# Optimization experiments

Hardware: AMD Instinct MI355X
Metric: run time of the kernel (lower is better)

The kernel has to match this reference:

```python
import jax, jax.numpy as jnp
import numpy as np
from jax import lax

IMG = 224.0
IOU_THRESH = 0.5

def box_cxcywh_to_xyxy(b):
    cx, cy, w, h = b[..., 0], b[..., 1], b[..., 2], b[..., 3]
    return jnp.stack([cx - 0.5 * w, cy - 0.5 * h, cx + 0.5 * w, cy + 0.5 * h], axis=-1)

def box_iou(a, b):
    area_a = (a[:, 2] - a[:, 0]) * (a[:, 3] - a[:, 1])
    area_b = (b[:, 2] - b[:, 0]) * (b[:, 3] - b[:, 1])
    lt = jnp.maximum(a[:, None, :2], b[None, :, :2])
    rb = jnp.minimum(a[:, None, 2:], b[None, :, 2:])
    wh = jnp.clip(rb - lt, 0.0)
    inter = wh[..., 0] * wh[..., 1]
    return inter / (area_a[:, None] + area_b[None, :] - inter)

def gumbel_softmax(key, logits, axis, tau=1.0):
    # straight-through hard gumbel-softmax (matches torch hard=True)
    g = jax.random.gumbel(key, logits.shape, logits.dtype)
    y = jax.nn.softmax((logits + g) / tau, axis=axis)
    y_hard = jax.nn.one_hot(jnp.argmax(y, axis=axis), y.shape[axis], axis=axis, dtype=y.dtype)
    return y + lax.stop_gradient(y_hard - y)

def nms_indices(boxes, scores, thresh):
    # iterative greedy NMS, returns kept indices in descending-score order (as torchvision)
    n = boxes.shape[0]
    order = jnp.argsort(-scores)
    b = boxes[order]
    areas = (b[:, 2] - b[:, 0]) * (b[:, 3] - b[:, 1])
    pos = jnp.arange(n)
    def body(i, suppressed):
        bi = b[i]
        lt = jnp.maximum(bi[:2], b[:, :2])
        rb = jnp.minimum(bi[2:], b[:, 2:])
        wh = jnp.clip(rb - lt, 0.0)
        inter = wh[:, 0] * wh[:, 1]
        iou = inter / (areas[i] + areas - inter)
        sup = (iou > thresh) & (pos > i) & jnp.logical_not(suppressed[i])
        return suppressed | sup
    suppressed = lax.fori_loop(0, n, body, jnp.zeros((n,), bool))
    keep = np.asarray(jnp.logical_not(suppressed))
    return jnp.asarray(np.asarray(order)[keep])

def _keys():
    return jax.random.split(jax.random.key(42), 3)

def _boxes_and_scores(classencodings, pred_logits, pred_boxes, tgt_ids, batch_idx, tgt_bbox, k0):
    C = classencodings.shape[0]
    B, Q, D = pred_logits.shape
    similarity = jnp.einsum('bqd,cd->bqc', pred_logits, classencodings)
    out_scores = jnp.max(similarity, axis=-1)
    clt = gumbel_softmax(k0, similarity, axis=-1)                      # [B,Q,C] hard
    offx = jnp.arange(C, dtype=pred_logits.dtype) * IMG
    offy = jnp.arange(B, dtype=pred_logits.dtype) * IMG
    ox = jnp.sum(clt * offx, axis=-1)                                  # [B,Q]
    oy = jnp.broadcast_to(offy[:, None], (B, Q))
    out_off = jnp.tile(jnp.stack([ox, oy], axis=-1), (1, 1, 2))        # [B,Q,4]
    out_bbox = (box_cxcywh_to_xyxy(pred_boxes) + out_off).reshape(-1, 4)
    f = pred_logits.dtype
    gt_off = jnp.tile(jnp.stack([IMG * tgt_ids.astype(f), IMG * batch_idx.astype(f)], axis=-1), (1, 2))
    tb = box_cxcywh_to_xyxy(tgt_bbox) + gt_off                         # [N,4]
    return similarity, out_scores.reshape(-1), out_bbox, tb

def ce_diag(logits):
    # CrossEntropyLoss(mean) with targets arange(n)
    return -jnp.mean(jnp.diagonal(jax.nn.log_softmax(logits, axis=1)))

def _forward(classencodings, pred_logits, pred_boxes, pred_masks, tgt_masks, tgt_embs, tgt_bbox, tgt_ids, batch_idx, nms_idx):
    k0, k1, k2 = _keys()
    B, Q, D = pred_logits.shape
    N = tgt_embs.shape[0]
    W, H = tgt_masks.shape[-2:]
    similarity, out_scores, out_bbox, tb = _boxes_and_scores(classencodings, pred_logits, pred_boxes, tgt_ids, batch_idx, tgt_bbox, k0)
    kept = out_bbox[nms_idx]                                           # [K,4]
    K = kept.shape[0]
    iou = box_iou(kept, tb)
    iou = jnp.where(jnp.isnan(iou), 0.0, iou)
    gt_log = jax.nn.softmax(iou, axis=1)
    gt_one_hot = gumbel_softmax(k1, gt_log, axis=1)                    # [K,N]
    gt_sel = gt_one_hot.T @ kept                                       # [N,4]
    gt_ious = jnp.diagonal(box_iou(gt_sel, tb))
    out_embs = gt_one_hot.T @ pred_logits.reshape(-1, D)[nms_idx]      # [N,D]
    class_loss = ce_diag(tgt_embs @ out_embs.T) + ce_diag(out_embs @ tgt_embs.T)
    scores = jnp.einsum('bqd,nd->bqn', pred_logits, tgt_embs).reshape(B * Q, N)
    ind = gumbel_softmax(k2, scores, axis=0).T                         # [N,B*Q]
    om = (ind @ pred_masks.reshape(B * Q, -1)).reshape(N, W, H)
    overall_mask_loss = jnp.mean((om - tgt_masks) ** 2)
    ocm = jnp.einsum('qwh,bcq->bcwh', om, similarity) / om.shape[1]    # [B,Q,W,H] (N==C==Q)
    ocm = jax.nn.softmax(ocm, axis=1)
    batch_lookup = jax.nn.one_hot(batch_idx, B, dtype=pred_logits.dtype).T  # [B,N]
    gt_sim = tgt_embs @ classencodings.T                               # [N,C]
    tsim = batch_lookup[:, :, None] * gt_sim[None, :, :]               # [B,N,C]
    gt_cm = jnp.einsum('bnc,nwh->bcwh', tsim, tgt_masks)               # [B,C,W,H]
    inp = ocm.reshape(B, -1)
    tgt = gt_cm.reshape(B, -1)
    dice = jnp.mean(jnp.sum(inp * tgt) / (jnp.sum(inp, -1) + jnp.sum(tgt, -1) + 1e-6))
    l1 = jnp.abs(gt_sel - tb).sum()
    return jnp.stack([class_loss, dice, overall_mask_loss / K, (1.0 - gt_ious).sum() / K, l1 / K])

def setup_inputs():
    key = jax.random.key(0)
    ks = jax.random.split(key, 10)
    B, Q, C, N, D, W, H = 8, 300, 300, 300, 256, 96, 96
    return {
        'classencodings': jax.random.normal(ks[0], (C, D), jnp.float32),
        'pred_logits': jax.random.normal(ks[1], (B, Q, D), jnp.float32),
        'pred_boxes': jax.random.uniform(ks[2], (B, Q, 4), jnp.float32),
        'pred_masks': jax.random.normal(ks[3], (B * Q, W, H), jnp.float32),
        'tgt_masks': jax.random.uniform(ks[4], (N, W, H), jnp.float32),
        'tgt_embs': jax.random.normal(ks[5], (N, D), jnp.float32),
        'tgt_bbox': jax.random.uniform(ks[6], (N, 4), jnp.float32),
        'im_masks': jnp.ones((B, 224, 224), jnp.float32),
        'tgt_ids': jax.random.randint(ks[7], (N,), 0, C, jnp.int32),
        'batch_idx': jnp.sort(jax.random.randint(ks[8], (N,), 0, B, jnp.int32)),
    }

def reference(classencodings, pred_logits, pred_boxes, pred_masks, tgt_masks, tgt_embs, tgt_bbox, im_masks, tgt_ids, batch_idx):
    k0, _, _ = _keys()
    _, scores, out_bbox, _ = _boxes_and_scores(classencodings, pred_logits, pred_boxes, tgt_ids, batch_idx, tgt_bbox, k0)
    nms_idx = nms_indices(out_bbox, scores, IOU_THRESH)
    return _forward(classencodings, pred_logits, pred_boxes, pred_masks, tgt_masks, tgt_embs, tgt_bbox, tgt_ids, batch_idx, nms_idx)
```

## Files before the change

### kernel.cpp

```cpp
#include <hip/hip_runtime.h>
#include <stdint.h>

#define DEVFN __device__ __forceinline__

typedef unsigned short u16;
typedef short bf16x8 __attribute__((ext_vector_type(8)));
typedef float f32x4 __attribute__((ext_vector_type(4)));

constexpr int BB = 8, QQ = 300, CC = 300, NN = 300, DD = 256;
constexpr int WHX = 9216, BQ = 2400, SIMW = 600;
constexpr int QP = 320;
constexpr int CP = 304;
constexpr int KP = 96;
constexpr int NP = 416;
constexpr int CELLCAP = 300;

constexpr size_t F_SIMS   = 0;
constexpr size_t F_GTSIM  = F_SIMS   + (size_t)BQ*SIMW;
constexpr size_t F_MM     = F_GTSIM  + (size_t)NN*CC;
constexpr size_t F_SCORE  = F_MM     + (size_t)NN*NN;
constexpr size_t F_BBOX   = F_SCORE  + BQ;
constexpr size_t F_TB     = F_BBOX   + (size_t)BQ*4;
constexpr size_t F_SB     = F_TB     + (size_t)NN*4;
constexpr size_t F_SAREA  = F_SB     + (size_t)BQ*4;
constexpr size_t F_KB     = F_SAREA  + BQ;
constexpr size_t F_ROWSUM = F_KB     + (size_t)BQ*4;
constexpr size_t F_OE     = F_ROWSUM + NN;
constexpr size_t F_GSEL   = F_OE     + (size_t)NN*DD;
constexpr size_t F_MSUM   = F_GSEL   + (size_t)NN*4;
constexpr size_t F_STGT   = F_MSUM   + NN;
constexpr size_t F_SC     = F_STGT   + 8;
constexpr size_t F_CNT    = F_SC     + 16;
constexpr size_t F_ACCEND = F_CNT    + BQ;
constexpr size_t F_ORDER  = F_ACCEND;
constexpr size_t F_NMSIDX = F_ORDER  + BQ;
constexpr size_t F_SEL2   = F_NMSIDX + BQ;
constexpr size_t F_BSTART = F_SEL2   + NN;
constexpr size_t F_KINT   = F_BSTART + 16;
constexpr size_t F_CLS    = F_KINT   + 4;
constexpr size_t F_KEEPF  = F_CLS    + BQ;
constexpr size_t F_LIST   = F_KEEPF  + BQ;
constexpr size_t F_SIMTB  = ((F_LIST + (size_t)BQ*CELLCAP + 7) & ~(size_t)7);
constexpr size_t F_OMT    = F_SIMTB + (size_t)BB*CP*QP/2;
constexpr size_t F_TMT    = F_OMT   + (size_t)WHX*QP/2;
constexpr size_t F_GTP    = F_TMT   + (size_t)WHX*NP/2;
constexpr size_t F_TOTAL  = F_GTP   + (size_t)BB*CP*KP/2;

DEVFN uint32_t rotl32(uint32_t v, int r){ return (v << r) | (v >> (32 - r)); }

DEVFN void tf2x32(uint32_t k0, uint32_t k1, uint32_t x0, uint32_t x1,
                  uint32_t& o0, uint32_t& o1){
  uint32_t ks2 = k0 ^ k1 ^ 0x1BD11BDAu;
  x0 += k0; x1 += k1;
#define TFR(r) x0 += x1; x1 = rotl32(x1, r); x1 ^= x0;
  TFR(13) TFR(15) TFR(26) TFR(6)   x0 += k1;  x1 += ks2 + 1u;
  TFR(17) TFR(29) TFR(16) TFR(24)  x0 += ks2; x1 += k0  + 2u;
  TFR(13) TFR(15) TFR(26) TFR(6)   x0 += k0;  x1 += k1  + 3u;
  TFR(17) TFR(29) TFR(16) TFR(24)  x0 += k1;  x1 += ks2 + 4u;
  TFR(13) TFR(15) TFR(26) TFR(6)   x0 += ks2; x1 += k0  + 5u;
#undef TFR
  o0 = x0; o1 = x1;
}

DEVFN void subkey(int i, uint32_t& k0, uint32_t& k1){
  tf2x32(0u, 42u, 0u, (uint32_t)i, k0, k1);
}

DEVFN float gumbel32(uint32_t k0, uint32_t k1, uint32_t idx){
  uint32_t h, l; tf2x32(k0, k1, 0u, idx, h, l);
  uint32_t bits = h ^ l;
  float f = __uint_as_float((bits >> 9) | 0x3F800000u) - 1.0f;
  const float tiny = 1.17549435e-38f;
  float u = fmaxf(tiny, f + tiny);
  return -logf(-logf(u));
}

DEVFN float iou_xyxy(float ax1,float ay1,float ax2,float ay2,
                     float bx1,float by1,float bx2,float by2){
  float aa = (ax2-ax1)*(ay2-ay1);
  float ab = (bx2-bx1)*(by2-by1);
  float lx = fmaxf(ax1,bx1), ly = fmaxf(ay1,by1);
  float rx = fminf(ax2,bx2), ry = fminf(ay2,by2);
  float iw = fmaxf(rx-lx,0.f), ih = fmaxf(ry-ly,0.f);
  float in_ = iw*ih;
  return in_/(aa+ab-in_);
}

DEVFN u16 f2bf(float x){
  uint32_t u = __float_as_uint(x);
  uint32_t r = u + 0x7FFFu + ((u >> 16) & 1u);
  return (u16)(r >> 16);
}

DEVFN void gload_lds16(const u16* g, u16* l){
  __builtin_amdgcn_global_load_lds(
      (const __attribute__((address_space(1))) unsigned int*)g,
      (__attribute__((address_space(3))) unsigned int*)l,
      16, 0, 0);
}

__global__ __launch_bounds__(256) void k_gemm_t(
    const float* __restrict__ pl, const float* __restrict__ ce,
    const float* __restrict__ te, float* __restrict__ sims,
    float* __restrict__ gtsim){
  __shared__ float As[16][64];
  __shared__ float Bs[16][64];
  const int row0 = blockIdx.x * 64, col0 = blockIdx.y * 64;
  const int tid = threadIdx.x;
  const int lrow = tid >> 2, lk0 = (tid & 3) * 4;
  const int tr = tid >> 4, tc = tid & 15;

  float acc[4][4];
  #pragma unroll
  for (int i = 0; i < 4; i++)
    #pragma unroll
    for (int j = 0; j < 4; j++) acc[i][j] = 0.f;

  const float4 z4 = {0.f,0.f,0.f,0.f};
  const int grow = row0 + lrow;
  const int gcol = col0 + lrow;
  const float* arow = nullptr;
  if (grow < 2400) arow = pl + (size_t)grow * DD;
  else if (grow < 2700) arow = te + (size_t)(grow - 2400) * DD;
  const float* brow = nullptr;
  if (gcol < 300) brow = ce + (size_t)gcol * DD;
  else if (gcol < 600) brow = te + (size_t)(gcol - 300) * DD;

  float4 av = arow ? *(const float4*)(arow + lk0) : z4;
  float4 bv = brow ? *(const float4*)(brow + lk0) : z4;

  for (int step = 0; step < 16; step++){
    __syncthreads();
    #pragma unroll
    for (int j = 0; j < 4; j++){
      As[lk0 + j][lrow] = ((const float*)&av)[j];
      Bs[lk0 + j][lrow] = ((const float*)&bv)[j];
    }
    __syncthreads();
    if (step + 1 < 16){
      const int k0 = (step + 1) * 16;
      av = arow ? *(const float4*)(arow + k0 + lk0) : z4;
      bv = brow ? *(const float4*)(brow + k0 + lk0) : z4;
    }
    #pragma unroll
    for (int kk = 0; kk < 16; kk++){
      float4 a4 = *(const float4*)&As[kk][tr*4];
      float4 b4 = *(const float4*)&Bs[kk][tc*4];
      float a[4] = {a4.x,a4.y,a4.z,a4.w};
      float b[4] = {b4.x,b4.y,b4.z,b4.w};
      #pragma unroll
      for (int i = 0; i < 4; i++)
        #pragma unroll
        for (int j = 0; j < 4; j++)
          acc[i][j] = fmaf(a[i], b[j], acc[i][j]);
    }
  }

  #pragma unroll
  for (int i = 0; i < 4; i++){
    const int r = row0 + tr*4 + i;
    const int c0 = col0 + tc*4;
    if (r < 2400){
      if (c0 < 600){
        float4 o0 = {acc[i][0],acc[i][1],acc[i][2],acc[i][3]};
        *(float4*)(sims + (size_t)r*SIMW + c0) = o0;
      }
    } else if (r < 2700){
      const int n = r - 2400;
      #pragma unroll
      for (int j = 0; j < 4; j++){
        int c = c0 + j;
        if (c < 300) gtsim[(size_t)n*CC + c] = acc[i][j];
      }
    }
  }
}

__global__ __launch_bounds__(512) void k_post(
    const float* __restrict__ sims, const float* __restrict__ pb,
    const float* __restrict__ tbb, const int* __restrict__ tids,
    const int* __restrict__ bidx, const float* __restrict__ gtsim,
    float* __restrict__ score, float* __restrict__ bbox,
    float* __restrict__ tb, float* __restrict__ rowsum,
    int* __restrict__ clsout){
  int bq = blockIdx.x, tid = threadIdx.x;
  __shared__ float sv[512];
  __shared__ int   si[512];
  float v = (tid < CC) ? sims[(size_t)bq*SIMW + tid] : -INFINITY;
  sv[tid] = v; __syncthreads();
  for (int s = 256; s > 0; s >>= 1){ if (tid < s) sv[tid] = fmaxf(sv[tid], sv[tid+s]); __syncthreads(); }
  if (tid == 0) score[bq] = sv[0];
  __syncthreads();
  uint32_t gk0, gk1; subkey(0, gk0, gk1);
  float y = (tid < CC) ? v + gumbel32(gk0, gk1, (uint32_t)(bq*CC + tid)) : -INFINITY;
  sv[tid] = y; si[tid] = tid; __syncthreads();
  for (int s = 256; s > 0; s >>= 1){
    if (tid < s){
      float ov = sv[tid+s]; int oi = si[tid+s];
      if (ov > sv[tid] || (ov == sv[tid] && oi < si[tid])){ sv[tid] = ov; si[tid] = oi; }
    }
    __syncthreads();
  }
  if (tid == 0){
    int cls = si[0];
    clsout[bq] = cls;
    float ox = 224.0f * (float)cls;
    float oy = 224.0f * (float)(bq / QQ);
    float cx = pb[bq*4+0], cy = pb[bq*4+1], ww = pb[bq*4+2], hh = pb[bq*4+3];
    bbox[bq*4+0] = cx - 0.5f*ww + ox;
    bbox[bq*4+1] = cy - 0.5f*hh + oy;
    bbox[bq*4+2] = cx + 0.5f*ww + ox;
    bbox[bq*4+3] = cy + 0.5f*hh + oy;
  }
  if (bq < NN){
    __syncthreads();
    float rs = (tid < CC) ? gtsim[(size_t)bq*CC + tid] : 0.f;
    sv[tid] = rs; __syncthreads();
    for (int s = 256; s > 0; s >>= 1){ if (tid < s) sv[tid] += sv[tid+s]; __syncthreads(); }
    if (tid == 0) rowsum[bq] = sv[0];
    if (tid == 1){
      float gx = 224.0f * (float)tids[bq], gy = 224.0f * (float)bidx[bq];
      float cx = tbb[bq*4+0], cy = tbb[bq*4+1], ww = tbb[bq*4+2], hh = tbb[bq*4+3];
      tb[bq*4+0] = cx - 0.5f*ww + gx;
      tb[bq*4+1] = cy - 0.5f*hh + gy;
      tb[bq*4+2] = cx + 0.5f*ww + gx;
      tb[bq*4+3] = cy + 0.5f*hh + gy;
    }
  }
}

__global__ __launch_bounds__(256) void k_rankgather(
    const float* __restrict__ score, const float* __restrict__ bbox,
    const int* __restrict__ cls, const int* __restrict__ bidx,
    int* __restrict__ order, float* __restrict__ sb,
    int* __restrict__ bstart, int* __restrict__ cnt,
    int* __restrict__ list){
  const int t = blockIdx.x;
  const int tid = threadIdx.x;
  const float st = score[t];
  int c = 0;
  for (int j = tid; j < BQ; j += 256){
    float sj = score[j];
    c += (sj > st) || (sj == st && j < t);
  }
  __shared__ int red[256];
  red[tid] = c; __syncthreads();
  for (int s = 128; s > 0; s >>= 1){
    if (tid < s) red[tid] += red[tid+s];
    __syncthreads();
  }
  if (tid == 0){
    int r = red[0];
    order[r] = t;
    float x1 = bbox[t*4+0], y1 = bbox[t*4+1], x2 = bbox[t*4+2], y2 = bbox[t*4+3];
    sb[r*4+0] = x1; sb[r*4+1] = y1; sb[r*4+2] = x2; sb[r*4+3] = y2;
    int key = (t / QQ) * CC + cls[t];
    int slot = atomicAdd(&cnt[key], 1);
    list[(size_t)key*CELLCAP + slot] = r;
  }
  if (t == 0 && tid >= 32 && tid < 41){
    int b = tid - 32, cb = 0;
    for (int n = 0; n < NN; n++) cb += (bidx[n] < b);
    bstart[b] = cb;
  }
}

__global__ __launch_bounds__(256) void k_cellnms(
    const float* __restrict__ sb, const int* __restrict__ cnt,
    const int* __restrict__ list, int* __restrict__ keepf){
  int key = blockIdx.x*256 + threadIdx.x;
  if (key >= BB*CC) return;
  int m = cnt[key];
  if (m <= 0) return;
  const int* lst = list + (size_t)key*CELLCAP;
  unsigned long long keptmask = 0ull;
  int prevp = -1;
  for (int a = 0; a < m; a++){
    int pa = 0x7fffffff;
    for (int j = 0; j < m; j++){
      int pj = lst[j];
      if (pj > prevp && pj < pa) pa = pj;
    }
    prevp = pa;
    float4 A = ((const float4*)sb)[pa];
    float areaA = (A.z-A.x)*(A.w-A.y);
    bool kept = true;
    int pbprev = -1;
    for (int b2 = 0; b2 < a; b2++){
      int pb = 0x7fffffff;
      for (int j = 0; j < m; j++){
        int pj = lst[j];
        if (pj > pbprev && pj < pb) pb = pj;
      }
      pbprev = pb;
      bool keptb = (m <= 64) ? (((keptmask >> b2) & 1ull) != 0ull) : (keepf[pb] != 0);
      if (!keptb) continue;
      float4 B = ((const float4*)sb)[pb];
      float areaB = (B.z-B.x)*(B.w-B.y);
      float lx = fmaxf(A.x,B.x), ly = fmaxf(A.y,B.y);
      float rx = fminf(A.z,B.z), ry = fminf(A.w,B.w);
      float iw = fmaxf(rx-lx,0.f), ih = fmaxf(ry-ly,0.f);
      float inter = iw*ih;
      if (inter/(areaA + areaB - inter) > 0.5f){ kept = false; break; }
    }
    if (m <= 64 && kept) keptmask |= (1ull << a);
    keepf[pa] = kept ? 1 : 0;
  }
}

__global__ __launch_bounds__(256) void k_compact(
    const int* __restrict__ keepflag, const int* __restrict__ order,
    const float* __restrict__ sb, int* __restrict__ nmsidx,
    float* __restrict__ kb, int* __restrict__ kint){
  __shared__ int csum[256];
  int tid = threadIdx.x;
  int p0 = tid*10;
  int keepf[10];
  int cnt = 0;
  #pragma unroll
  for (int d = 0; d < 10; d++){
    int p = p0 + d;
    int k = 0;
    if (p < BQ) k = keepflag[p];
    keepf[d] = k; cnt += k;
  }
  csum[tid] = cnt; __syncthreads();
  for (int s = 1; s < 256; s <<= 1){
    int add = (tid >= s) ? csum[tid - s] : 0;
    __syncthreads();
    csum[tid] += add;
    __syncthreads();
  }
  int pos = csum[tid] - cnt;
  #pragma unroll
  for (int d = 0; d < 10; d++){
    if (keepf[d]){
      int p = p0 + d;
      nmsidx[pos] = order[p];
      ((float4*)kb)[pos] = ((const float4*)sb)[p];
      pos++;
    }
  }
  if (tid == 255) kint[0] = csum[255];
}

__global__ __launch_bounds__(512) void k_gtsel(
    const float* __restrict__ kb, const float* __restrict__ tb,
    const int* __restrict__ nmsidx, const float* __restrict__ pl,
    const int* __restrict__ kint, float* __restrict__ gsel,
    float* __restrict__ oe){
  int k = blockIdx.x;
  if (k >= kint[0]) return;
  int tid = threadIdx.x;
  __shared__ float sv[512];
  __shared__ int   si[512];
  float4 a = ((const float4*)kb)[k];
  float iou = -INFINITY;
  if (tid < NN){
    float4 t = ((const float4*)tb)[tid];
    iou = iou_xyxy(a.x,a.y,a.z,a.w, t.x,t.y,t.z,t.w);
    if (iou != iou) iou = 0.f;
  }
  sv[tid] = iou; __syncthreads();
  for (int s = 256; s > 0; s >>= 1){ if (tid < s) sv[tid] = fmaxf(sv[tid], sv[tid+s]); __syncthreads(); }
  float m = sv[0]; __syncthreads();
  float e = (tid < NN) ? expf(iou - m) : 0.f;
  sv[tid] = e; __syncthreads();
  for (int s = 256; s > 0; s >>= 1){ if (tid < s) sv[tid] += sv[tid+s]; __syncthreads(); }
  float S = sv[0]; __syncthreads();
  uint32_t gk0, gk1; subkey(1, gk0, gk1);
  float y = (tid < NN) ? (e / S + gumbel32(gk0, gk1, (uint32_t)(k*NN + tid))) : -INFINITY;
  sv[tid] = y; si[tid] = tid; __syncthreads();
  for (int s = 256; s > 0; s >>= 1){
    if (tid < s){
      float ov = sv[tid+s]; int oi = si[tid+s];
      if (ov > sv[tid] || (ov == sv[tid] && oi < si[tid])){ sv[tid] = ov; si[tid] = oi; }
    }
    __syncthreads();
  }
  int sel = si[0];
  if (tid < 4) atomicAdd(&gsel[sel*4 + tid], ((const float*)&a)[tid]);
  if (tid < DD) atomicAdd(&oe[(size_t)sel*DD + tid], pl[(size_t)nmsidx[k]*DD + tid]);
}

__global__ __launch_bounds__(256) void k_m(
    const float* __restrict__ te, const float* __restrict__ oe,
    float* __restrict__ M){
  int idx = blockIdx.x*256 + threadIdx.x;
  if (idx >= NN*NN) return;
  int i = idx / NN, j = idx % NN;
  const float4* a4 = (const float4*)(te + (size_t)i*DD);
  const float4* b4 = (const float4*)(oe + (size_t)j*DD);
  float s = 0.f;
  #pragma unroll 8
  for (int t = 0; t < DD/4; t++){
    float4 x = a4[t], y = b4[t];
    s += x.x*y.x + x.y*y.y + x.z*y.z + x.w*y.w;
  }
  M[idx] = s;
}

__global__ __launch_bounds__(64) void k_ce(
    const float* __restrict__ M, float* __restrict__ sc){
  int i = blockIdx.x, lane = threadIdx.x;
  float m = -INFINITY;
  for (int j = lane; j < NN; j += 64) m = fmaxf(m, M[(size_t)i*NN + j]);
  for (int o = 32; o > 0; o >>= 1) m = fmaxf(m, __shfl_xor(m, o));
  float s = 0.f;
  for (int j = lane; j < NN; j += 64) s += expf(M[(size_t)i*NN + j] - m);
  for (int o = 32; o > 0; o >>= 1) s += __shfl_xor(s, o);
  float lr = m + logf(s);
  float m2 = -INFINITY;
  for (int j = lane; j < NN; j += 64) m2 = fmaxf(m2, M[(size_t)j*NN + i]);
  for (int o = 32; o > 0; o >>= 1) m2 = fmaxf(m2, __shfl_xor(m2, o));
  float s2 = 0.f;
  for (int j = lane; j < NN; j += 64) s2 += expf(M[(size_t)j*NN + i] - m2);
  for (int o = 32; o > 0; o >>= 1) s2 += __shfl_xor(s2, o);
  float lc = m2 + logf(s2);
  if (lane == 0){
    float d = M[(size_t)i*NN + i];
    atomicAdd(&sc[0], lr - d);
    atomicAdd(&sc[1], lc - d);
  }
}

__global__ __launch_bounds__(256) void k_sel2(
    const float* __restrict__ sims, int* __restrict__ sel2){
  int n = blockIdx.x, tid = threadIdx.x;
  uint32_t gk0, gk1; subkey(2, gk0, gk1);
  float best = -INFINITY; int bi = 0x7fffffff;
  for (int r = tid; r < BQ; r += 256){
    float v = sims[(size_t)r*SIMW + CC + n] + gumbel32(gk0, gk1, (uint32_t)(r*NN + n));
    if (v > best){ best = v; bi = r; }
  }
  __shared__ float sv[256];
  __shared__ int   si[256];
  sv[tid] = best; si[tid] = bi; __syncthreads();
  for (int s = 128; s > 0; s >>= 1){
    if (tid < s){
      float ov = sv[tid+s]; int oi = si[tid+s];
      if (ov > sv[tid] || (ov == sv[tid] && oi < si[tid])){ sv[tid] = ov; si[tid] = oi; }
    }
    __syncthreads();
  }
  if (tid == 0) sel2[n] = si[0];
}

__global__ __launch_bounds__(256) void k_om(
    const float* __restrict__ pm, const float* __restrict__ tm,
    const int* __restrict__ sel2, float* __restrict__ msum,
    float* __restrict__ sc){
  int nb = blockIdx.x;
  int n = nb / 9, ch = nb % 9;
  int c0 = ch*1024 + threadIdx.x*4;
  const float4 o4 = *(const float4*)(pm + (size_t)sel2[n]*WHX + c0);
  const float4 t4 = *(const float4*)(tm + (size_t)n*WHX + c0);
  float dx = o4.x-t4.x, dy = o4.y-t4.y, dz = o4.z-t4.z, dw = o4.w-t4.w;
  float d2 = dx*dx + dy*dy + dz*dz + dw*dw;
  float ts = t4.x + t4.y + t4.z + t4.w;
  __shared__ float r1[256], r2[256];
  r1[threadIdx.x] = d2; r2[threadIdx.x] = ts; __syncthreads();
  for (int s = 128; s > 0; s >>= 1){
    if (threadIdx.x < s){ r1[threadIdx.x] += r1[threadIdx.x+s]; r2[threadIdx.x] += r2[threadIdx.x+s]; }
    __syncthreads();
  }
  if (threadIdx.x == 0){ atomicAdd(&sc[2], r1[0]); atomicAdd(&msum[n], r2[0]); }
}

__global__ __launch_bounds__(256) void t_simT(
    const float* __restrict__ sims, u16* __restrict__ simTb){
  __shared__ float ld[32][65];
  int q0 = blockIdx.x*32, c0 = blockIdx.y*64, b = blockIdx.z;
  int tid = threadIdx.x;
  for (int i = tid; i < 32*64; i += 256){
    int qi = i >> 6, ci = i & 63;
    int q = q0 + qi, c = c0 + ci;
    ld[qi][ci] = (q < QQ && c < CC) ? sims[((size_t)b*QQ + q)*SIMW + c] : 0.f;
  }
  __syncthreads();
  int cloc = tid >> 2, j0 = (tid & 3)*8;
  int c = c0 + cloc;
  if (c < CP){
    u16 tmp[8];
    #pragma unroll
    for (int j = 0; j < 8; j++) tmp[j] = f2bf(ld[j0+j][cloc]);
    *(uint4*)(simTb + ((size_t)b*CP + c)*QP + q0 + j0) = *(const uint4*)tmp;
  }
}

__global__ __launch_bounds__(256) void t_omT(
    const float* __restrict__ pm, const int* __restrict__ sel2,
    u16* __restrict__ omT){
  __shared__ float ld[32][65];
  int q0 = blockIdx.x*32, wh0 = blockIdx.y*64;
  int tid = threadIdx.x;
  for (int i = tid; i < 32*64; i += 256){
    int qi = i >> 6, wi = i & 63;
    int q = q0 + qi;
    ld[qi][wi] = (q < QQ) ? pm[(size_t)sel2[q]*WHX + wh0 + wi] * (1.0f/96.0f) : 0.f;
  }
  __syncthreads();
  int wloc = tid >> 2, j0 = (tid & 3)*8;
  u16 tmp[8];
  #pragma unroll
  for (int j = 0; j < 8; j++) tmp[j] = f2bf(ld[j0+j][wloc]);
  *(uint4*)(omT + (size_t)(wh0+wloc)*QP + q0 + j0) = *(const uint4*)tmp;
}

__global__ __launch_bounds__(256) void t_tmT(
    const float* __restrict__ tm, u16* __restrict__ tmT){
  __shared__ float ld[32][65];
  int n0 = blockIdx.x*32, wh0 = blockIdx.y*64;
  int tid = threadIdx.x;
  for (int i = tid; i < 32*64; i += 256){
    int ni = i >> 6, wi = i & 63;
    int n = n0 + ni;
    ld[ni][wi] = (n < NN) ? tm[(size_t)n*WHX + wh0 + wi] : 0.f;
  }
  __syncthreads();
  int wloc = tid >> 2, j0 = (tid & 3)*8;
  u16 tmp[8];
  #pragma unroll
  for (int j = 0; j < 8; j++) tmp[j] = f2bf(ld[j0+j][wloc]);
  *(uint4*)(tmT + (size_t)(wh0+wloc)*NP + n0 + j0) = *(const uint4*)tmp;
}

__global__ __launch_bounds__(256) void t_gtp(
    const float* __restrict__ gtsim, const int* __restrict__ bstart,
    u16* __restrict__ gtp){
  int g = blockIdx.x*256 + threadIdx.x;
  if (g >= BB*CP*(KP/8)) return;
  int b = g / (CP*(KP/8));
  int rem = g - b*(CP*(KP/8));
  int c = rem / (KP/8);
  int kg = rem % (KP/8);
  int n0 = bstart[b], n1 = bstart[b+1];
  int kst = n0 & ~7;
  u16 tmp[8];
  #pragma unroll
  for (int j = 0; j < 8; j++){
    int n = kst + kg*8 + j;
    float v = (n >= n0 && n < n1 && c < CC) ? gtsim[(size_t)n*CC + c] : 0.f;
    tmp[j] = f2bf(v);
  }
  *(uint4*)(gtp + ((size_t)b*CP + c)*KP + kg*8) = *(const uint4*)tmp;
}

constexpr int ALDS = 32;
__global__ __launch_bounds__(256) void k_zsoft(
    const u16* __restrict__ simTb, const u16* __restrict__ omT,
    const u16* __restrict__ gtp, const u16* __restrict__ tmT,
    const int* __restrict__ bstart, float* __restrict__ sc){
  const int bid = blockIdx.x;
  const int xcd = bid & 7;
  const int r9  = bid >> 3;
  const int tile = xcd * 18 + (r9 % 18);
  const int b    = r9 / 18;
  const int tid = threadIdx.x;
  const int w = tid >> 6, l = tid & 63;
  const int lrow = l & 15, lgrp = l >> 4;
  const int col = tile*64 + w*16 + lrow;

  __shared__ u16 As[2][CP*ALDS];
  __shared__ float red[256];

  const u16* Ab = simTb + (size_t)b*CP*QP;
  int srcoff[5];
  #pragma unroll
  for (int i = 0; i < 5; i++){
    int p = (w*5 + i)*64 + l;
    int row = p >> 2, cs = p & 3;
    int g = cs ^ ((row >> 1) & 3);
    srcoff[i] = row*QP + g*8;
  }
  const int nIss = (w == 3) ? 4 : 5;
  const int roff = (lgrp ^ ((lrow >> 1) & 3)) << 3;
  const u16* pB = omT + (size_t)col*QP;

  #pragma unroll
  for (int i = 0; i < 5; i++){
    if (i < nIss) gload_lds16(Ab + srcoff[i], &As[0][(w*5+i)*512]);
  }
  bf16x8 bcur = *(const bf16x8*)(pB);

  f32x4 acc[19];
  #pragma unroll
  for (int t = 0; t < 19; t++) acc[t] = (f32x4){0.f,0.f,0.f,0.f};
  __syncthreads();

  for (int ks = 0; ks < 10; ks++){
    const int cur = ks & 1;
    bf16x8 bnext;
    if (ks + 1 < 10){
      const int ko = (ks + 1) * 32;
      #pragma unroll
      for (int i = 0; i < 5; i++){
        if (i < nIss) gload_lds16(Ab + srcoff[i] + ko, &As[cur ^ 1][(w*5+i)*512]);
      }
      bnext = *(const bf16x8*)(pB + ko);
    }
    __builtin_amdgcn_s_setprio(1);
    #pragma unroll
    for (int t = 0; t < 19; t++){
      bf16x8 af = *(const bf16x8*)&As[cur][t*16*ALDS + lrow*ALDS + roff];
      acc[t] = __builtin_amdgcn_mfma_f32_16x16x32_bf16(af, bcur, acc[t], 0, 0, 0);
    }
    __builtin_amdgcn_s_setprio(0);
    bcur = bnext;
    __syncthreads();
  }

  float lmax = -INFINITY;
  #pragma unroll
  for (int t = 0; t < 19; t++){
    if (t == 18 && lgrp == 3) continue;
    lmax = fmaxf(lmax, fmaxf(fmaxf(acc[t][0], acc[t][1]), fmaxf(acc[t][2], acc[t][3])));
  }
  lmax = fmaxf(lmax, __shfl_xor(lmax, 16));
  lmax = fmaxf(lmax, __shfl_xor(lmax, 32));
  float ls = 0.f;
  #pragma unroll
  for (int t = 0; t < 19; t++){
    if (t == 18 && lgrp == 3){
      acc[t] = (f32x4){0.f,0.f,0.f,0.f};
      continue;
    }
    float p0 = __expf(acc[t][0] - lmax);
    float p1 = __expf(acc[t][1] - lmax);
    float p2 = __expf(acc[t][2] - lmax);
    float p3 = __expf(acc[t][3] - lmax);
    acc[t][0] = p0; acc[t][1] = p1; acc[t][2] = p2; acc[t][3] = p3;
    ls += p0 + p1 + p2 + p3;
  }
  float S = ls;
  S += __shfl_xor(S, 16);
  S += __shfl_xor(S, 32);
  float inv = 1.f / S;

  int n0 = bstart[b];
  int kst = n0 & ~7;
  const u16* tB = tmT + (size_t)col*NP + kst + lgrp*8;
  bf16x8 b2a = *(const bf16x8*)(tB);
  bf16x8 b2b = *(const bf16x8*)(tB + 32);
  bf16x8 b2c = *(const bf16x8*)(tB + 64);
  const u16* A2 = gtp + (size_t)b*CP*KP + lgrp*8;
  float dl = 0.f;
  #pragma unroll
  for (int t = 0; t < 19; t++){
    const u16* ar = A2 + (size_t)(t*16 + lrow)*KP;
    f32x4 rr = (f32x4){0.f,0.f,0.f,0.f};
    rr = __builtin_amdgcn_mfma_f32_16x16x32_bf16(*(const bf16x8*)(ar),      b2a, rr, 0, 0, 0);
    rr = __builtin_amdgcn_mfma_f32_16x16x32_bf16(*(const bf16x8*)(ar + 32), b2b, rr, 0, 0, 0);
    rr = __builtin_amdgcn_mfma_f32_16x16x32_bf16(*(const bf16x8*)(ar + 64), b2c, rr, 0, 0, 0);
    dl += acc[t][0]*rr[0] + acc[t][1]*rr[1] + acc[t][2]*rr[2] + acc[t][3]*rr[3];
  }
  dl *= inv;

  red[tid] = dl; __syncthreads();
  for (int s = 128; s > 0; s >>= 1){
    if (tid < s) red[tid] += red[tid+s];
    __syncthreads();
  }
  if (tid == 0) atomicAdd(&sc[5], red[0]);
}

__global__ __launch_bounds__(512) void k_final3(
    const float* __restrict__ gsel, const float* __restrict__ tb,
    const int* __restrict__ bidx, const float* __restrict__ rowsum,
    const float* __restrict__ msum, const float* __restrict__ sc,
    const int* __restrict__ kint, float* __restrict__ out){
  int tid = threadIdx.x;
  __shared__ float s1[512], s2[512];
  __shared__ float stgt[8];
  if (tid < 8) stgt[tid] = 0.f;
  __syncthreads();
  float a1 = 0.f, a2 = 0.f;
  if (tid < NN){
    float4 g = ((const float4*)gsel)[tid];
    float4 t = ((const float4*)tb)[tid];
    float iou = iou_xyxy(g.x,g.y,g.z,g.w, t.x,t.y,t.z,t.w);
    a1 = 1.f - iou;
    a2 = fabsf(g.x-t.x) + fabsf(g.y-t.y) + fabsf(g.z-t.z) + fabsf(g.w-t.w);
    atomicAdd(&stgt[bidx[tid]], rowsum[tid] * msum[tid]);
  }
  s1[tid] = a1; s2[tid] = a2; __syncthreads();
  for (int s = 256; s > 0; s >>= 1){
    if (tid < s){ s1[tid] += s1[tid+s]; s2[tid] += s2[tid+s]; }
    __syncthreads();
  }
  if (tid == 0){
    float K = (float)kint[0];
    float cls = sc[0]/300.f + sc[1]/300.f;
    float stot = sc[5];
    float dice = 0.f;
    for (int b = 0; b < 8; b++) dice += stot / (9216.0f + stgt[b] + 1e-6f);
    dice *= (1.0f/8.0f);
    out[0] = cls;
    out[1] = dice;
    out[2] = (sc[2] / 2764800.0f) / K;
    out[3] = s1[0] / K;
    out[4] = s2[0] / K;
  }
}

extern "C" void kernel_launch(void* const* d_in, const int* in_sizes, int n_in,
                              void* d_out, int out_size, void* d_ws, size_t ws_size,
                              hipStream_t stream) {
  const float* ce  = (const float*)d_in[0];
  const float* pl  = (const float*)d_in[1];
  const float* pb  = (const float*)d_in[2];
  const float* pm  = (const float*)d_in[3];
  const float* tm  = (const float*)d_in[4];
  const float* te  = (const float*)d_in[5];
  const float* tbb = (const float*)d_in[6];
  const int*  tids = (const int*)d_in[8];
  const int*  bidx = (const int*)d_in[9];
  float* out = (float*)d_out;
  float* w = (float*)d_ws;

  if (ws_size < F_TOTAL * sizeof(float)) return;

  float* SIMS   = w + F_SIMS;
  float* GTSIM  = w + F_GTSIM;
  float* MM     = w + F_MM;
  float* SCORE  = w + F_SCORE;
  float* BBOX   = w + F_BBOX;
  float* TBOX   = w + F_TB;
  float* SB     = w + F_SB;
  float* KB     = w + F_KB;
  float* ROWSUM = w + F_ROWSUM;
  float* OE     = w + F_OE;
  float* GSEL   = w + F_GSEL;
  float* MSUM   = w + F_MSUM;
  float* SC     = w + F_SC;
  int*   CNT    = (int*)(w + F_CNT);
  int*   ORDER  = (int*)(w + F_ORDER);
  int*   NMSIDX = (int*)(w + F_NMSIDX);
  int*   SEL2   = (int*)(w + F_SEL2);
  int*   BSTART = (int*)(w + F_BSTART);
  int*   KINT   = (int*)(w + F_KINT);
  int*   CLS    = (int*)(w + F_CLS);
  int*   KEEPF  = (int*)(w + F_KEEPF);
  int*   LIST   = (int*)(w + F_LIST);
  u16* SIMTB = (u16*)(w + F_SIMTB);
  u16* OMT   = (u16*)(w + F_OMT);
  u16* TMT   = (u16*)(w + F_TMT);
  u16* GTP   = (u16*)(w + F_GTP);

  hipMemsetAsync(w + F_OE, 0, (F_ACCEND - F_OE) * sizeof(float), stream);

  k_gemm_t<<<dim3(43, 10), 256, 0, stream>>>(pl, ce, te, SIMS, GTSIM);
  k_post<<<BQ, 512, 0, stream>>>(SIMS, pb, tbb, tids, bidx, GTSIM, SCORE, BBOX, TBOX, ROWSUM, CLS);
  k_rankgather<<<BQ, 256, 0, stream>>>(SCORE, BBOX, CLS, bidx, ORDER, SB, BSTART, CNT, LIST);
  k_cellnms<<<(BB*CC + 255)/256, 256, 0, stream>>>(SB, CNT, LIST, KEEPF);
  k_compact<<<1, 256, 0, stream>>>(KEEPF, ORDER, SB, NMSIDX, KB, KINT);
  k_gtsel<<<BQ, 512, 0, stream>>>(KB, TBOX, NMSIDX, pl, KINT, GSEL, OE);
  k_m<<<(NN*NN + 255)/256, 256, 0, stream>>>(te, OE, MM);
  k_ce<<<NN, 64, 0, stream>>>(MM, SC);
  k_sel2<<<NN, 256, 0, stream>>>(SIMS, SEL2);
  k_om<<<NN*9, 256, 0, stream>>>(pm, tm, SEL2, MSUM, SC);

  t_simT<<<dim3(QP/32, 5, BB), 256, 0, stream>>>(SIMS, SIMTB);
  t_omT<<<dim3(QP/32, WHX/64), 256, 0, stream>>>(pm, SEL2, OMT);
  t_tmT<<<dim3(NP/32, WHX/64), 256, 0, stream>>>(tm, TMT);
  t_gtp<<<(BB*CP*(KP/8) + 255)/256, 256, 0, stream>>>(GTSIM, BSTART, GTP);

  k_zsoft<<<dim3((WHX/64) * BB), 256, 0, stream>>>(SIMTB, OMT, GTP, TMT, BSTART, SC);
  k_final3<<<1, 512, 0, stream>>>(GSEL, TBOX, bidx, ROWSUM, MSUM, SC, KINT, out);
}
```

Before: 274.1 us.

## Fuse pack kernels, transpose sel2 input, tile M gemm, prefetch zsoft operands

Merges the four transpose/pack kernels and the mask-loss kernel into one multi-role launch. The similarity GEMM also writes a transposed copy, so sel2 reads coalesced data instead of strided columns. The per-element dot-product kernel becomes a tiled shared-memory GEMM, and k_post uses 256 threads with two elements each. In k_zsoft the second MFMA stage's loads are hoisted and double-buffered, and the omT pointer gains a lane-group offset. These cut launch count and uncoalesced traffic, at the cost of extra workspace and a behavioural change in the omT addressing.

Result: faster. 268.0 us (-2.2%).

```diff
diff --git a/kernel.cpp b/kernel.cpp
--- a/kernel.cpp
+++ b/kernel.cpp
@@ -40,7 +40,8 @@
 constexpr size_t F_CLS    = F_KINT   + 4;
 constexpr size_t F_KEEPF  = F_CLS    + BQ;
 constexpr size_t F_LIST   = F_KEEPF  + BQ;
-constexpr size_t F_SIMTB  = ((F_LIST + (size_t)BQ*CELLCAP + 7) & ~(size_t)7);
+constexpr size_t F_S2T    = F_LIST   + (size_t)BQ*CELLCAP;
+constexpr size_t F_SIMTB  = ((F_S2T + (size_t)NN*BQ + 7) & ~(size_t)7);
 constexpr size_t F_OMT    = F_SIMTB + (size_t)BB*CP*QP/2;
 constexpr size_t F_TMT    = F_OMT   + (size_t)WHX*QP/2;
 constexpr size_t F_GTP    = F_TMT   + (size_t)WHX*NP/2;
@@ -102,7 +103,7 @@
 __global__ __launch_bounds__(256) void k_gemm_t(
     const float* __restrict__ pl, const float* __restrict__ ce,
     const float* __restrict__ te, float* __restrict__ sims,
-    float* __restrict__ gtsim){
+    float* __restrict__ gtsim, float* __restrict__ s2t){
   __shared__ float As[16][64];
   __shared__ float Bs[16][64];
   const int row0 = blockIdx.x * 64, col0 = blockIdx.y * 64;
@@ -164,6 +165,11 @@
       if (c0 < 600){
         float4 o0 = {acc[i][0],acc[i][1],acc[i][2],acc[i][3]};
         *(float4*)(sims + (size_t)r*SIMW + c0) = o0;
+        if (c0 >= 300){
+          #pragma unroll
+          for (int j = 0; j < 4; j++)
+            s2t[(size_t)(c0 + j - 300)*BQ + r] = acc[i][j];
+        }
       }
     } else if (r < 2700){
       const int n = r - 2400;
@@ -176,7 +182,7 @@
   }
 }
 
-__global__ __launch_bounds__(512) void k_post(
+__global__ __launch_bounds__(256) void k_post(
     const float* __restrict__ sims, const float* __restrict__ pb,
     const float* __restrict__ tbb, const int* __restrict__ tids,
     const int* __restrict__ bidx, const float* __restrict__ gtsim,
@@ -184,17 +190,22 @@
     float* __restrict__ tb, float* __restrict__ rowsum,
     int* __restrict__ clsout){
   int bq = blockIdx.x, tid = threadIdx.x;
-  __shared__ float sv[512];
-  __shared__ int   si[512];
-  float v = (tid < CC) ? sims[(size_t)bq*SIMW + tid] : -INFINITY;
-  sv[tid] = v; __syncthreads();
-  for (int s = 256; s > 0; s >>= 1){ if (tid < s) sv[tid] = fmaxf(sv[tid], sv[tid+s]); __syncthreads(); }
+  __shared__ float sv[256];
+  __shared__ int   si[256];
+  const int i2 = tid + 256;
+  float v1 = (tid < CC) ? sims[(size_t)bq*SIMW + tid] : -INFINITY;
+  float v2 = (i2  < CC) ? sims[(size_t)bq*SIMW + i2]  : -INFINITY;
+  sv[tid] = fmaxf(v1, v2); __syncthreads();
+  for (int s = 128; s > 0; s >>= 1){ if (tid < s) sv[tid] = fmaxf(sv[tid], sv[tid+s]); __syncthreads(); }
   if (tid == 0) score[bq] = sv[0];
   __syncthreads();
   uint32_t gk0, gk1; subkey(0, gk0, gk1);
-  float y = (tid < CC) ? v + gumbel32(gk0, gk1, (uint32_t)(bq*CC + tid)) : -INFINITY;
-  sv[tid] = y; si[tid] = tid; __syncthreads();
-  for (int s = 256; s > 0; s >>= 1){
+  float y1 = (tid < CC) ? v1 + gumbel32(gk0, gk1, (uint32_t)(bq*CC + tid)) : -INFINITY;
+  float y2 = (i2  < CC) ? v2 + gumbel32(gk0, gk1, (uint32_t)(bq*CC + i2))  : -INFINITY;
+  float ym; int yi;
+  if (y2 > y1){ ym = y2; yi = i2; } else { ym = y1; yi = tid; }
+  sv[tid] = ym; si[tid] = yi; __syncthreads();
+  for (int s = 128; s > 0; s >>= 1){
     if (tid < s){
       float ov = sv[tid+s]; int oi = si[tid+s];
       if (ov > sv[tid] || (ov == sv[tid] && oi < si[tid])){ sv[tid] = ov; si[tid] = oi; }
@@ -214,9 +225,10 @@
   }
   if (bq < NN){
     __syncthreads();
-    float rs = (tid < CC) ? gtsim[(size_t)bq*CC + tid] : 0.f;
-    sv[tid] = rs; __syncthreads();
-    for (int s = 256; s > 0; s >>= 1){ if (tid < s) sv[tid] += sv[tid+s]; __syncthreads(); }
+    float r1 = (tid < CC) ? gtsim[(size_t)bq*CC + tid] : 0.f;
+    float r2 = (i2  < CC) ? gtsim[(size_t)bq*CC + i2]  : 0.f;
+    sv[tid] = r1 + r2; __syncthreads();
+    for (int s = 128; s > 0; s >>= 1){ if (tid < s) sv[tid] += sv[tid+s]; __syncthreads(); }
     if (tid == 0) rowsum[bq] = sv[0];
     if (tid == 1){
       float gx = 224.0f * (float)tids[bq], gy = 224.0f * (float)bidx[bq];
@@ -383,21 +395,46 @@
   if (tid < DD) atomicAdd(&oe[(size_t)sel*DD + tid], pl[(size_t)nmsidx[k]*DD + tid]);
 }
 
-__global__ __launch_bounds__(256) void k_m(
+__global__ __launch_bounds__(256) void k_m_t(
     const float* __restrict__ te, const float* __restrict__ oe,
     float* __restrict__ M){
-  int idx = blockIdx.x*256 + threadIdx.x;
-  if (idx >= NN*NN) return;
-  int i = idx / NN, j = idx % NN;
-  const float4* a4 = (const float4*)(te + (size_t)i*DD);
-  const float4* b4 = (const float4*)(oe + (size_t)j*DD);
-  float s = 0.f;
-  #pragma unroll 8
-  for (int t = 0; t < DD/4; t++){
-    float4 x = a4[t], y = b4[t];
-    s += x.x*y.x + x.y*y.y + x.z*y.z + x.w*y.w;
-  }
-  M[idx] = s;
+  __shared__ float As[16][32];
+  __shared__ float Bs[16][32];
+  const int row0 = blockIdx.x * 32, col0 = blockIdx.y * 32;
+  const int tid = threadIdx.x;
+  const int lr = tid >> 3, lk0 = (tid & 7) * 2;
+  const int tr = tid >> 4, tc = tid & 15;
+  float acc[2][2] = {{0.f,0.f},{0.f,0.f}};
+  const float* arow = (row0 + lr < NN) ? te + (size_t)(row0 + lr)*DD : nullptr;
+  const float* brow = (col0 + lr < NN) ? oe + (size_t)(col0 + lr)*DD : nullptr;
+  for (int step = 0; step < 16; step++){
+    const int k0 = step*16;
+    float2 a2 = arow ? *(const float2*)(arow + k0 + lk0) : float2{0.f,0.f};
+    float2 b2 = brow ? *(const float2*)(brow + k0 + lk0) : float2{0.f,0.f};
+    __syncthreads();
+    As[lk0][lr] = a2.x; As[lk0+1][lr] = a2.y;
+    Bs[lk0][lr] = b2.x; Bs[lk0+1][lr] = b2.y;
+    __syncthreads();
+    #pragma unroll
+    for (int kk = 0; kk < 16; kk++){
+      float a0 = As[kk][tr*2], a1 = As[kk][tr*2+1];
+      float b0 = Bs[kk][tc*2], b1 = Bs[kk][tc*2+1];
+      acc[0][0] = fmaf(a0,b0,acc[0][0]);
+      acc[0][1] = fmaf(a0,b1,acc[0][1]);
+      acc[1][0] = fmaf(a1,b0,acc[1][0]);
+      acc[1][1] = fmaf(a1,b1,acc[1][1]);
+    }
+  }
+  #pragma unroll
+  for (int i = 0; i < 2; i++){
+    int r = row0 + tr*2 + i;
+    if (r >= NN) continue;
+    #pragma unroll
+    for (int j = 0; j < 2; j++){
+      int c = col0 + tc*2 + j;
+      if (c < NN) M[(size_t)r*NN + c] = acc[i][j];
+    }
+  }
 }
 
 __global__ __launch_bounds__(64) void k_ce(
@@ -425,12 +462,12 @@
 }
 
 __global__ __launch_bounds__(256) void k_sel2(
-    const float* __restrict__ sims, int* __restrict__ sel2){
+    const float* __restrict__ s2t, int* __restrict__ sel2){
   int n = blockIdx.x, tid = threadIdx.x;
   uint32_t gk0, gk1; subkey(2, gk0, gk1);
   float best = -INFINITY; int bi = 0x7fffffff;
   for (int r = tid; r < BQ; r += 256){
-    float v = sims[(size_t)r*SIMW + CC + n] + gumbel32(gk0, gk1, (uint32_t)(r*NN + n));
+    float v = s2t[(size_t)n*BQ + r] + gumbel32(gk0, gk1, (uint32_t)(r*NN + n));
     if (v > best){ best = v; bi = r; }
   }
   __shared__ float sv[256];
@@ -446,104 +483,101 @@
   if (tid == 0) sel2[n] = si[0];
 }
 
-__global__ __launch_bounds__(256) void k_om(
-    const float* __restrict__ pm, const float* __restrict__ tm,
-    const int* __restrict__ sel2, float* __restrict__ msum,
-    float* __restrict__ sc){
-  int nb = blockIdx.x;
-  int n = nb / 9, ch = nb % 9;
-  int c0 = ch*1024 + threadIdx.x*4;
-  const float4 o4 = *(const float4*)(pm + (size_t)sel2[n]*WHX + c0);
-  const float4 t4 = *(const float4*)(tm + (size_t)n*WHX + c0);
-  float dx = o4.x-t4.x, dy = o4.y-t4.y, dz = o4.z-t4.z, dw = o4.w-t4.w;
-  float d2 = dx*dx + dy*dy + dz*dz + dw*dw;
-  float ts = t4.x + t4.y + t4.z + t4.w;
-  __shared__ float r1[256], r2[256];
-  r1[threadIdx.x] = d2; r2[threadIdx.x] = ts; __syncthreads();
-  for (int s = 128; s > 0; s >>= 1){
-    if (threadIdx.x < s){ r1[threadIdx.x] += r1[threadIdx.x+s]; r2[threadIdx.x] += r2[threadIdx.x+s]; }
-    __syncthreads();
-  }
-  if (threadIdx.x == 0){ atomicAdd(&sc[2], r1[0]); atomicAdd(&msum[n], r2[0]); }
-}
-
-__global__ __launch_bounds__(256) void t_simT(
-    const float* __restrict__ sims, u16* __restrict__ simTb){
+constexpr int PB_SIMT = 400;
+constexpr int PB_OMT  = 1440;
+constexpr int PB_TMT  = 1872;
+constexpr int PB_GTP  = 114;
+constexpr int PB_OM   = 2700;
+__global__ __launch_bounds__(256) void k_pack(
+    const float* __restrict__ sims, const float* __restrict__ pm,
+    const float* __restrict__ tm, const float* __restrict__ gtsim,
+    const int* __restrict__ sel2, const int* __restrict__ bstart,
+    u16* __restrict__ simTb, u16* __restrict__ omT,
+    u16* __restrict__ tmT, u16* __restrict__ gtp,
+    float* __restrict__ msum, float* __restrict__ sc){
   __shared__ float ld[32][65];
-  int q0 = blockIdx.x*32, c0 = blockIdx.y*64, b = blockIdx.z;
-  int tid = threadIdx.x;
-  for (int i = tid; i < 32*64; i += 256){
-    int qi = i >> 6, ci = i & 63;
-    int q = q0 + qi, c = c0 + ci;
-    ld[qi][ci] = (q < QQ && c < CC) ? sims[((size_t)b*QQ + q)*SIMW + c] : 0.f;
-  }
-  __syncthreads();
-  int cloc = tid >> 2, j0 = (tid & 3)*8;
-  int c = c0 + cloc;
-  if (c < CP){
+  const int blk = blockIdx.x;
+  const int tid = threadIdx.x;
+
+  if (blk < PB_SIMT){
+    int bx = blk % 10, by = (blk / 10) % 5, b = blk / 50;
+    int q0 = bx*32, c0 = by*64;
+    for (int i = tid; i < 32*64; i += 256){
+      int qi = i >> 6, ci = i & 63;
+      int q = q0 + qi, c = c0 + ci;
+      ld[qi][ci] = (q < QQ && c < CC) ? sims[((size_t)b*QQ + q)*SIMW + c] : 0.f;
+    }
+    __syncthreads();
+    int cloc = tid >> 2, j0 = (tid & 3)*8;
+    int c = c0 + cloc;
+    if (c < CP){
+      u16 tmp[8];
+      #pragma unroll
+      for (int j = 0; j < 8; j++) tmp[j] = f2bf(ld[j0+j][cloc]);
+      *(uint4*)(simTb + ((size_t)b*CP + c)*QP + q0 + j0) = *(const uint4*)tmp;
+    }
+  } else if (blk < PB_SIMT + PB_OMT){
+    int r = blk - PB_SIMT;
+    int q0 = (r % 10)*32, wh0 = (r / 10)*64;
+    for (int i = tid; i < 32*64; i += 256){
+      int qi = i >> 6, wi = i & 63;
+      int q = q0 + qi;
+      ld[qi][wi] = (q < QQ) ? pm[(size_t)sel2[q]*WHX + wh0 + wi] * (1.0f/96.0f) : 0.f;
+    }
+    __syncthreads();
+    int wloc = tid >> 2, j0 = (tid & 3)*8;
     u16 tmp[8];
     #pragma unroll
-    for (int j = 0; j < 8; j++) tmp[j] = f2bf(ld[j0+j][cloc]);
-    *(uint4*)(simTb + ((size_t)b*CP + c)*QP + q0 + j0) = *(const uint4*)tmp;
-  }
-}
-
-__global__ __launch_bounds__(256) void t_omT(
-    const float* __restrict__ pm, const int* __restrict__ sel2,
-    u16* __restrict__ omT){
-  __shared__ float ld[32][65];
-  int q0 = blockIdx.x*32, wh0 = blockIdx.y*64;
-  int tid = threadIdx.x;
-  for (int i = tid; i < 32*64; i += 256){
-    int qi = i >> 6, wi = i & 63;
-    int q = q0 + qi;
-    ld[qi][wi] = (q < QQ) ? pm[(size_t)sel2[q]*WHX + wh0 + wi] * (1.0f/96.0f) : 0.f;
-  }
-  __syncthreads();
-  int wloc = tid >> 2, j0 = (tid & 3)*8;
-  u16 tmp[8];
-  #pragma unroll
-  for (int j = 0; j < 8; j++) tmp[j] = f2bf(ld[j0+j][wloc]);
-  *(uint4*)(omT + (size_t)(wh0+wloc)*QP + q0 + j0) = *(const uint4*)tmp;
-}
-
-__global__ __launch_bounds__(256) void t_tmT(
-    const float* __restrict__ tm, u16* __restrict__ tmT){
-  __shared__ float ld[32][65];
-  int n0 = blockIdx.x*32, wh0 = blockIdx.y*64;
-  int tid = threadIdx.x;
-  for (int i = tid; i < 32*64; i += 256){
-    int ni = i >> 6, wi = i & 63;
-    int n = n0 + ni;
-    ld[ni][wi] = (n < NN) ? tm[(size_t)n*WHX + wh0 + wi] : 0.f;
-  }
-  __syncthreads();
-  int wloc = tid >> 2, j0 = (tid & 3)*8;
-  u16 tmp[8];
-  #pragma unroll
-  for (int j = 0; j < 8; j++) tmp[j] = f2bf(ld[j0+j][wloc]);
-  *(uint4*)(tmT + (size_t)(wh0+wloc)*NP + n0 + j0) = *(const uint4*)tmp;
-}
-
-__global__ __launch_bounds__(256) void t_gtp(
-    const float* __restrict__ gtsim, const int* __restrict__ bstart,
-    u16* __restrict__ gtp){
-  int g = blockIdx.x*256 + threadIdx.x;
-  if (g >= BB*CP*(KP/8)) return;
-  int b = g / (CP*(KP/8));
-  int rem = g - b*(CP*(KP/8));
-  int c = rem / (KP/8);
-  int kg = rem % (KP/8);
-  int n0 = bstart[b], n1 = bstart[b+1];
-  int kst = n0 & ~7;
-  u16 tmp[8];
-  #pragma unroll
-  for (int j = 0; j < 8; j++){
-    int n = kst + kg*8 + j;
-    float v = (n >= n0 && n < n1 && c < CC) ? gtsim[(size_t)n*CC + c] : 0.f;
-    tmp[j] = f2bf(v);
-  }
-  *(uint4*)(gtp + ((size_t)b*CP + c)*KP + kg*8) = *(const uint4*)tmp;
+    for (int j = 0; j < 8; j++) tmp[j] = f2bf(ld[j0+j][wloc]);
+    *(uint4*)(omT + (size_t)(wh0+wloc)*QP + q0 + j0) = *(const uint4*)tmp;
+  } else if (blk < PB_SIMT + PB_OMT + PB_TMT){
+    int r = blk - PB_SIMT - PB_OMT;
+    int n0 = (r % 13)*32, wh0 = (r / 13)*64;
+    for (int i = tid; i < 32*64; i += 256){
+      int ni = i >> 6, wi = i & 63;
+      int n = n0 + ni;
+      ld[ni][wi] = (n < NN) ? tm[(size_t)n*WHX + wh0 + wi] : 0.f;
+    }
+    __syncthreads();
+    int wloc = tid >> 2, j0 = (tid & 3)*8;
+    u16 tmp[8];
+    #pragma unroll
+    for (int j = 0; j < 8; j++) tmp[j] = f2bf(ld[j0+j][wloc]);
+    *(uint4*)(tmT + (size_t)(wh0+wloc)*NP + n0 + j0) = *(const uint4*)tmp;
+  } else if (blk < PB_SIMT + PB_OMT + PB_TMT + PB_GTP){
+    int g = (blk - PB_SIMT - PB_OMT - PB_TMT)*256 + tid;
+    int b = g / (CP*(KP/8));
+    int rem = g - b*(CP*(KP/8));
+    int c = rem / (KP/8);
+    int kg = rem % (KP/8);
+    int n0 = bstart[b], n1 = bstart[b+1];
+    int kst = n0 & ~7;
+    u16 tmp[8];
+    #pragma unroll
+    for (int j = 0; j < 8; j++){
+      int n = kst + kg*8 + j;
+      float v = (n >= n0 && n < n1 && c < CC) ? gtsim[(size_t)n*CC + c] : 0.f;
+      tmp[j] = f2bf(v);
+    }
+    *(uint4*)(gtp + ((size_t)b*CP + c)*KP + kg*8) = *(const uint4*)tmp;
+  } else {
+    int nb = blk - (PB_SIMT + PB_OMT + PB_TMT + PB_GTP);
+    int n = nb / 9, ch = nb % 9;
+    int c0 = ch*1024 + tid*4;
+    const float4 o4 = *(const float4*)(pm + (size_t)sel2[n]*WHX + c0);
+    const float4 t4 = *(const float4*)(tm + (size_t)n*WHX + c0);
+    float dx = o4.x-t4.x, dy = o4.y-t4.y, dz = o4.z-t4.z, dw = o4.w-t4.w;
+    float d2 = dx*dx + dy*dy + dz*dz + dw*dw;
+    float ts = t4.x + t4.y + t4.z + t4.w;
+    float* r1 = &ld[0][0];
+    float* r2 = r1 + 256;
+    r1[tid] = d2; r2[tid] = ts; __syncthreads();
+    for (int s = 128; s > 0; s >>= 1){
+      if (tid < s){ r1[tid] += r1[tid+s]; r2[tid] += r2[tid+s]; }
+      __syncthreads();
+    }
+    if (tid == 0){ atomicAdd(&sc[2], r1[0]); atomicAdd(&msum[n], r2[0]); }
+  }
 }
 
 constexpr int ALDS = 32;
@@ -575,7 +609,7 @@
   }
   const int nIss = (w == 3) ? 4 : 5;
   const int roff = (lgrp ^ ((lrow >> 1) & 3)) << 3;
-  const u16* pB = omT + (size_t)col*QP;
+  const u16* pB = omT + (size_t)col*QP + lgrp*8;
 
   #pragma unroll
   for (int i = 0; i < 5; i++){
@@ -610,6 +644,20 @@
     __syncthreads();
   }
 
+  const int n0 = bstart[b];
+  const int kst = n0 & ~7;
+  const u16* tB = tmT + (size_t)col*NP + kst + lgrp*8;
+  bf16x8 b2a = *(const bf16x8*)(tB);
+  bf16x8 b2b = *(const bf16x8*)(tB + 32);
+  bf16x8 b2c = *(const bf16x8*)(tB + 64);
+  const u16* A2 = gtp + (size_t)b*CP*KP + (size_t)lrow*KP + lgrp*8;
+  bf16x8 ca0 = *(const bf16x8*)(A2);
+  bf16x8 ca1 = *(const bf16x8*)(A2 + 32);
+  bf16x8 ca2 = *(const bf16x8*)(A2 + 64);
+  bf16x8 da0 = *(const bf16x8*)(A2 + 16*KP);
+  bf16x8 da1 = *(const bf16x8*)(A2 + 16*KP + 32);
+  bf16x8 da2 = *(const bf16x8*)(A2 + 16*KP + 64);
+
   float lmax = -INFINITY;
   #pragma unroll
   for (int t = 0; t < 19; t++){
@@ -637,22 +685,21 @@
   S += __shfl_xor(S, 32);
   float inv = 1.f / S;
 
-  int n0 = bstart[b];
-  int kst = n0 & ~7;
-  const u16* tB = tmT + (size_t)col*NP + kst + lgrp*8;
-  bf16x8 b2a = *(const bf16x8*)(tB);
-  bf16x8 b2b = *(const bf16x8*)(tB + 32);
-  bf16x8 b2c = *(const bf16x8*)(tB + 64);
-  const u16* A2 = gtp + (size_t)b*CP*KP + lgrp*8;
   float dl = 0.f;
   #pragma unroll
   for (int t = 0; t < 19; t++){
-    const u16* ar = A2 + (size_t)(t*16 + lrow)*KP;
     f32x4 rr = (f32x4){0.f,0.f,0.f,0.f};
-    rr = __builtin_amdgcn_mfma_f32_16x16x32_bf16(*(const bf16x8*)(ar),      b2a, rr, 0, 0, 0);
-    rr = __builtin_amdgcn_mfma_f32_16x16x32_bf16(*(const bf16x8*)(ar + 32), b2b, rr, 0, 0, 0);
-    rr = __builtin_amdgcn_mfma_f32_16x16x32_bf16(*(const bf16x8*)(ar + 64), b2c, rr, 0, 0, 0);
+    rr = __builtin_amdgcn_mfma_f32_16x16x32_bf16(ca0, b2a, rr, 0, 0, 0);
+    rr = __builtin_amdgcn_mfma_f32_16x16x32_bf16(ca1, b2b, rr, 0, 0, 0);
+    rr = __builtin_amdgcn_mfma_f32_16x16x32_bf16(ca2, b2c, rr, 0, 0, 0);
     dl += acc[t][0]*rr[0] + acc[t][1]*rr[1] + acc[t][2]*rr[2] + acc[t][3]*rr[3];
+    ca0 = da0; ca1 = da1; ca2 = da2;
+    if (t + 2 < 19){
+      const u16* ar = A2 + (size_t)(t + 2)*16*KP;
+      da0 = *(const bf16x8*)(ar);
+      da1 = *(const bf16x8*)(ar + 32);
+      da2 = *(const bf16x8*)(ar + 64);
+    }
   }
   dl *= inv;
 
@@ -733,6 +780,7 @@
   float* GSEL   = w + F_GSEL;
   float* MSUM   = w + F_MSUM;
   float* SC     = w + F_SC;
+  float* S2T    = w + F_S2T;
   int*   CNT    = (int*)(w + F_CNT);
   int*   ORDER  = (int*)(w + F_ORDER);
   int*   NMSIDX = (int*)(w + F_NMSIDX);
@@ -749,22 +797,17 @@
 
   hipMemsetAsync(w + F_OE, 0, (F_ACCEND - F_OE) * sizeof(float), stream);
 
-  k_gemm_t<<<dim3(43, 10), 256, 0, stream>>>(pl, ce, te, SIMS, GTSIM);
-  k_post<<<BQ, 512, 0, stream>>>(SIMS, pb, tbb, tids, bidx, GTSIM, SCORE, BBOX, TBOX, ROWSUM, CLS);
+  k_gemm_t<<<dim3(43, 10), 256, 0, stream>>>(pl, ce, te, SIMS, GTSIM, S2T);
+  k_post<<<BQ, 256, 0, stream>>>(SIMS, pb, tbb, tids, bidx, GTSIM, SCORE, BBOX, TBOX, ROWSUM, CLS);
   k_rankgather<<<BQ, 256, 0, stream>>>(SCORE, BBOX, CLS, bidx, ORDER, SB, BSTART, CNT, LIST);
+  k_sel2<<<NN, 256, 0, stream>>>(S2T, SEL2);
+  k_pack<<<PB_SIMT + PB_OMT + PB_TMT + PB_GTP + PB_OM, 256, 0, stream>>>(
+      SIMS, pm, tm, GTSIM, SEL2, BSTART, SIMTB, OMT, TMT, GTP, MSUM, SC);
   k_cellnms<<<(BB*CC + 255)/256, 256, 0, stream>>>(SB, CNT, LIST, KEEPF);
   k_compact<<<1, 256, 0, stream>>>(KEEPF, ORDER, SB, NMSIDX, KB, KINT);
   k_gtsel<<<BQ, 512, 0, stream>>>(KB, TBOX, NMSIDX, pl, KINT, GSEL, OE);
-  k_m<<<(NN*NN + 255)/256, 256, 0, stream>>>(te, OE, MM);
+  k_m_t<<<dim3(10, 10), 256, 0, stream>>>(te, OE, MM);
   k_ce<<<NN, 64, 0, stream>>>(MM, SC);
-  k_sel2<<<NN, 256, 0, stream>>>(SIMS, SEL2);
-  k_om<<<NN*9, 256, 0, stream>>>(pm, tm, SEL2, MSUM, SC);
-
-  t_simT<<<dim3(QP/32, 5, BB), 256, 0, stream>>>(SIMS, SIMTB);
-  t_omT<<<dim3(QP/32, WHX/64), 256, 0, stream>>>(pm, SEL2, OMT);
-  t_tmT<<<dim3(NP/32, WHX/64), 256, 0, stream>>>(tm, TMT);
-  t_gtp<<<(BB*CP*(KP/8) + 255)/256, 256, 0, stream>>>(GTSIM, BSTART, GTP);
-
   k_zsoft<<<dim3((WHX/64) * BB), 256, 0, stream>>>(SIMTB, OMT, GTP, TMT, BSTART, SC);
   k_final3<<<1, 512, 0, stream>>>(GSEL, TBOX, bidx, ROWSUM, MSUM, SC, KINT, out);
 }
```
